# Optimization experiments

Hardware: AMD Instinct MI355X
Metric: run time of the kernel (lower is better)

The kernel has to match this reference:

```python
import jax, jax.numpy as jnp
import numpy as np
from jax.scipy.special import gammaln, logsumexp

NEG = -1e9  # finite large-negative to keep gradients NaN-free


def setup_inputs() -> dict:
    key = jax.random.key(0)
    ks = jax.random.split(key, 8)
    B, T, D, C, K = 8, 4096, 64, 32, 20
    features = jax.random.normal(ks[0], (B, T, D), dtype=jnp.float32)
    # valid lengths in [T//2, T] so every sequence is long relative to K
    lengths = jax.random.randint(ks[1], (B,), T // 2, T + 1)
    poisson_log_rates = jax.random.normal(ks[2], (C,), dtype=jnp.float32) * 0.1 + jnp.log(8.0)
    gaussian_means = jax.random.normal(ks[3], (C, D), dtype=jnp.float32) * 0.5
    # tied diagonal covariance (as produced by initialize_gaussian / tied_diag)
    gaussian_cov = jnp.diag(jax.random.uniform(ks[4], (D,), minval=0.5, maxval=1.5))
    transition_logits = jax.random.normal(ks[5], (C, C), dtype=jnp.float32) * 0.1
    init_logits = jax.random.uniform(ks[6], (C,), dtype=jnp.float32)
    return dict(features=features, poisson_log_rates=poisson_log_rates,
                gaussian_means=gaussian_means, gaussian_cov=gaussian_cov,
                transition_logits=transition_logits, init_logits=init_logits,
                lengths=lengths, max_k=K)


def reference(features, poisson_log_rates, gaussian_means, gaussian_cov,
              transition_logits, init_logits, lengths, max_k):
    B, T, D = features.shape
    C = gaussian_means.shape[0]
    K = int(max_k)

    # ---- emission log-probs: tied full-covariance Gaussian per class -> (B,T,C)
    prec = jnp.linalg.inv(gaussian_cov)
    _, logdet = jnp.linalg.slogdet(gaussian_cov)
    xP = features @ prec                                        # (B,T,D)
    quad = jnp.einsum('btd,btd->bt', xP, features)              # x^T P x
    cross = jnp.einsum('btd,cd->btc', xP, gaussian_means)       # x^T P mu
    muPmu = jnp.einsum('cd,de,ce->c', gaussian_means, prec, gaussian_means)
    const = D * jnp.log(2.0 * jnp.pi) + logdet
    emit = -0.5 * (quad[:, :, None] - 2.0 * cross + muPmu[None, None, :] + const)  # (B,T,C)

    # ---- Poisson duration scores for d = 1..K -> (K,C)
    d = jnp.arange(1, K + 1, dtype=jnp.float32)[:, None]
    length_scores = d * poisson_log_rates[None, :] - jnp.exp(poisson_log_rates)[None, :] - gammaln(d + 1.0)

    # ---- normalized transition (to <- from, softmax over 'to' axis) and init
    trans = jax.nn.log_softmax(transition_logits, axis=0)       # trans[to, from]
    init = jax.nn.log_softmax(init_logits)

    # ---- span emission sums via cumsum differences (== sliding_sum windows)
    cum = jnp.concatenate([jnp.zeros((B, 1, C), emit.dtype), jnp.cumsum(emit, axis=1)], axis=1)  # (B,T+1,C)
    t_idx = jnp.arange(1, T + 1)[:, None]                        # (T,1) span end (exclusive)
    d_idx = jnp.arange(1, K + 1)[None, :]                        # (1,K) duration
    start = jnp.clip(t_idx - d_idx, 0, None)                     # (T,K) span start
    span = cum[:, t_idx, :] - cum[:, start, :]                   # (B,T,K,C)
    seg = span + length_scores[None, None, :, :]                 # add duration scores
    seg = jnp.transpose(seg, (1, 2, 0, 3))                       # (T,K,B,C)
    dur_valid = (d_idx <= t_idx)                                 # (T,K): need d <= t
    seg = jnp.where(dur_valid[:, :, None, None], seg, NEG)

    # ---- semi-Markov forward recursion over time.
    # buf[i] = alpha_star[t-1-i]; alpha_star[s][c] = best-sum of paths ending a
    # segment at s, already including the transition into the next label c.
    buf0 = jnp.full((K, B, C), NEG, emit.dtype).at[0].set(jnp.broadcast_to(init, (B, C)))

    def step(buf, seg_t):
        alpha_t = logsumexp(buf + seg_t, axis=0)                               # (B,C)
        astar = logsumexp(alpha_t[:, None, :] + trans[None, :, :], axis=2)     # (B,C)
        buf = jnp.concatenate([astar[None], buf[:-1]], axis=0)
        return buf, alpha_t

    _, alphas = jax.lax.scan(step, buf0, seg)                    # (T,B,C)
    logZ = logsumexp(alphas[lengths - 1, jnp.arange(B), :], axis=-1)
    return -logZ  # negative log marginal likelihood per sequence
```

## Files before the change

kernel.cpp:

```cpp
#include <hip/hip_runtime.h>
#include <math.h>

#define TT 4096
#define DD 64
#define CC 32
#define KK 20
#define TPE 4128
#define L2E 1.44269504088896340736f
#define LN2f 0.69314718055994530942f
#define PIN 10.0f

#if __has_builtin(__builtin_amdgcn_permlane32_swap)
#define HAVE_PLSWAP 1
#endif
#if __has_builtin(__builtin_amdgcn_permlane16_swap)
#define HAVE_PL16 1
#endif

__device__ __align__(16) float g_pmu[32 * 64];
__device__ __align__(16) float g_p2[64];
__device__ __align__(16) float g_mc[32];
__device__ __align__(16) float g_ls2[20 * 32];
__device__ __align__(16) float g_T[32 * 32];
__device__ __align__(16) float g_init2[32];
__device__ float g_mb;
__device__ __align__(16) float g_eT[8 * 32 * TPE];

__device__ __forceinline__ float fexp2(float x) {
#if __has_builtin(__builtin_amdgcn_exp2f)
    return __builtin_amdgcn_exp2f(x);
#else
    return __exp2f(x);
#endif
}
__device__ __forceinline__ float flog2(float x) {
#if __has_builtin(__builtin_amdgcn_logf)
    return __builtin_amdgcn_logf(x);
#else
    return __log2f(x);
#endif
}

#define RF(x) __int_as_float(__builtin_amdgcn_readfirstlane(__float_as_int(x)))

__device__ __forceinline__ float xswap32(float x) {
#ifdef HAVE_PLSWAP
    int xi = __float_as_int(x);
    auto pr = __builtin_amdgcn_permlane32_swap(xi, xi, false, false);
    int r0 = ((const int*)&pr)[0];
    int r1 = ((const int*)&pr)[1];
    return (r0 == xi) ? __int_as_float(r1) : __int_as_float(r0);
#else
    return __shfl_xor(x, 32);
#endif
}
__device__ __forceinline__ float xswap16(float x) {
#ifdef HAVE_PL16
    int xi = __float_as_int(x);
    auto pr = __builtin_amdgcn_permlane16_swap(xi, xi, false, false);
    int r0 = ((const int*)&pr)[0];
    int r1 = ((const int*)&pr)[1];
    return (r0 == xi) ? __int_as_float(r1) : __int_as_float(r0);
#else
    return __shfl_xor(x, 16);
#endif
}

#define DPPF(dst, src, CTRL) \
    dst = __int_as_float(__builtin_amdgcn_update_dpp(0, __float_as_int(src), (CTRL), 0xF, 0xF, 1))

__device__ __forceinline__ float wmax64(float x) {
    float m = x, t;
    DPPF(t, m, 0xB1);  m = fmaxf(m, t);
    DPPF(t, m, 0x4E);  m = fmaxf(m, t);
    DPPF(t, m, 0x141); m = fmaxf(m, t);
    DPPF(t, m, 0x140); m = fmaxf(m, t);
    m = fmaxf(m, xswap16(m));
    m = fmaxf(m, xswap32(m));
    return m;
}

__global__ void smm_setup(const float* __restrict__ plr,
                          const float* __restrict__ mu,
                          const float* __restrict__ cov,
                          const float* __restrict__ tl,
                          const float* __restrict__ il) {
    int l = threadIdx.x;
    __shared__ float red[64];
    __shared__ float redp[64];
    __shared__ float muP[32];
    __shared__ float constc_s;
    float cd = cov[l * 64 + l];
    float pd = 1.0f / cd;
    red[l] = logf(cd);
    redp[l] = pd;
    __syncthreads();
    if (l == 0) {
        float s = 0.f;
        for (int i = 0; i < 64; ++i) s += red[i];
        constc_s = 64.0f * logf(2.0f * 3.14159265358979323846f) + s;
    }
    __syncthreads();
    float constc = constc_s;

    g_p2[l] = 0.5f * L2E * pd;
    for (int c2 = 0; c2 < 32; ++c2)
        g_pmu[c2 * 64 + l] = L2E * pd * mu[c2 * 64 + l];

    if (l < 32) {
        float s = 0.f;
        for (int d2 = 0; d2 < 64; ++d2) {
            float m_ = mu[l * 64 + d2];
            s += m_ * m_ / cov[d2 * 64 + d2];
        }
        g_mc[l] = -0.5f * L2E * (s + constc);
        muP[l] = s;
    }
    for (int idx = l; idx < KK * CC; idx += 64) {
        int k = idx >> 5, c2 = idx & 31;
        float lr = plr[c2];
        g_ls2[idx] = L2E * ((float)(k + 1) * lr - expf(lr) - lgammaf((float)(k + 2)));
    }
    if (l < 32) {
        int from = l;
        float mx = -1e30f;
        for (int to = 0; to < 32; ++to) mx = fmaxf(mx, tl[to * 32 + from]);
        float s = 0.f;
        for (int to = 0; to < 32; ++to) s += expf(tl[to * 32 + from] - mx);
        float inv = 1.0f / s;
        for (int to = 0; to < 32; ++to)
            g_T[to * 32 + from] = expf(tl[to * 32 + from] - mx) * inv;
    }
    if (l == 32) {
        float mx = -1e30f;
        for (int c2 = 0; c2 < 32; ++c2) mx = fmaxf(mx, il[c2]);
        float s = 0.f;
        for (int c2 = 0; c2 < 32; ++c2) s += expf(il[c2] - mx);
        float lse = mx + logf(s);
        for (int c2 = 0; c2 < 32; ++c2) g_init2[c2] = L2E * (il[c2] - lse);
    }
    __syncthreads();
    if (l == 0) {
        float trP = 0.f;
        for (int i = 0; i < 64; ++i) trP += redp[i];
        float mm = 0.f;
        for (int c2 = 0; c2 < 32; ++c2) mm += muP[c2];
        mm *= (1.0f / 32.0f);
        g_mb = -0.5f * L2E * (constc + trP + mm);
    }
}

__global__ __launch_bounds__(256) void smm_emit(const float* __restrict__ feat) {
    int tid = threadIdx.x;
    int c = tid & 31, tl_ = tid >> 5;
    int t = blockIdx.x * 8 + tl_;
    int b = blockIdx.y;
    const float4* x4 = (const float4*)(feat + ((size_t)b * TT + t) * DD);
    const float4* pm4 = (const float4*)(g_pmu + c * 64);
    const float4* p24 = (const float4*)g_p2;
    float acc = g_mc[c];
#pragma unroll
    for (int i = 0; i < 16; ++i) {
        float4 xv = x4[i], pm = pm4[i], pv = p24[i];
        acc = fmaf(pm.x, xv.x, acc); acc = fmaf(-pv.x * xv.x, xv.x, acc);
        acc = fmaf(pm.y, xv.y, acc); acc = fmaf(-pv.y * xv.y, xv.y, acc);
        acc = fmaf(pm.z, xv.z, acc); acc = fmaf(-pv.z * xv.z, xv.z, acc);
        acc = fmaf(pm.w, xv.w, acc); acc = fmaf(-pv.w * xv.w, xv.w, acc);
    }
    float ev = fexp2(acc - g_mb);
    __shared__ float stage[32][9];
    stage[c][tl_] = ev;
    __syncthreads();
    int c2 = tid >> 3, j = tid & 7;
    int t0 = blockIdx.x * 8;
    int ti = (t0 + j + TT - 1) & (TT - 1);
    g_eT[((size_t)b * 32 + c2) * TPE + ti] = stage[c2][j];
}

#define GMV(PF, OUT)                                                              \
    {                                                                             \
        float G1, G2, G3, G7, G15;                                                \
        DPPF(G1, PF, 0xB1); DPPF(G2, PF, 0x4E); DPPF(G3, PF, 0x1B);               \
        DPPF(G7, PF, 0x141); DPPF(G15, PF, 0x140);                                \
        float G4, G5, G6, G8, G12, G13, G14;                                      \
        DPPF(G6, G1, 0x141); DPPF(G5, G2, 0x141); DPPF(G4, G3, 0x141);            \
        DPPF(G8, G7, 0x140); DPPF(G14, G1, 0x140); DPPF(G13, G2, 0x140);          \
        DPPF(G12, G3, 0x140);                                                     \
        float G9, G10, G11;                                                       \
        DPPF(G9, G14, 0x141); DPPF(G10, G13, 0x141); DPPF(G11, G12, 0x141);       \
        float a0 = Tr[0]*(PF); a0 = fmaf(Tr[1],G1,a0);   a0 = fmaf(Tr[2],G2,a0);   a0 = fmaf(Tr[3],G3,a0);    \
        float a1 = Tr[4]*G4;   a1 = fmaf(Tr[5],G5,a1);   a1 = fmaf(Tr[6],G6,a1);   a1 = fmaf(Tr[7],G7,a1);    \
        float a2 = Tr[8]*G8;   a2 = fmaf(Tr[9],G9,a2);   a2 = fmaf(Tr[10],G10,a2); a2 = fmaf(Tr[11],G11,a2);  \
        float a3 = Tr[12]*G12; a3 = fmaf(Tr[13],G13,a3); a3 = fmaf(Tr[14],G14,a3); a3 = fmaf(Tr[15],G15,a3);  \
        float accl_ = (a0 + a1) + (a2 + a3);                                      \
        OUT = accl_ + xswap16(xswap32(accl_));                                    \
    }

#define STEPS(EV, tcur)                                                           \
    {                                                                             \
        float pf = fmaf(accf, nu, OFF);                                           \
        float naccf;                                                              \
        GMV(pf, naccf)                                                            \
        pfc = pf;                                                                 \
        if ((tcur) == lenm1) { pfL = pf; refL = refc; }                           \
        float sg = (EV) * su;                                                     \
        float u2 = accf * nu;                                                     \
        float s0 = half ? Wc : u2;                                                \
        float e9 = z9 * sg;                                                       \
        float t9 = e9 * rr;                                                       \
        float x9 = xswap32(t9);                                                   \
        float Wn = half ? x9 : t9;                                                \
        z9 = z8*sg; z8 = z7*sg; z7 = z6*sg; z6 = z5*sg; z5 = z4*sg;               \
        z4 = z3*sg; z3 = z2*sg; z2 = z1*sg; z1 = s0*sg;                           \
        float tA = Pw1*z1; tA = fmaf(Pw2,z2,tA); tA = fmaf(Pw3,z3,tA);            \
        tA = fmaf(Pw4,z4,tA); tA = fmaf(Pw5,z5,tA);                               \
        float tB = Pw6*z6; tB = fmaf(Pw7,z7,tB); tB = fmaf(Pw8,z8,tB);            \
        tB = fmaf(Pw9,z9,tB);                                                     \
        float S = tA + tB;                                                        \
        float Sx = xswap32(S);                                                    \
        OFF = fmaxf((S + Sx) + Wn, 1e-36f);                                       \
        nu = sg * E1;                                                             \
        accf = naccf;                                                             \
        Wc = Wn;                                                                  \
        refc += (double)r8;                                                       \
    }

#define STEPM(EV)                                                                 \
    {                                                                             \
        float pf = fmaf(accf, nu, OFF);                                           \
        float naccf;                                                              \
        GMV(pf, naccf)                                                            \
        pfc = pf;                                                                 \
        float sg = (EV) * su;                                                     \
        float u2 = accf * nu;                                                     \
        float s0 = half ? Wc : u2;                                                \
        float e9 = z9 * sg;                                                       \
        float t9 = e9 * rr;                                                       \
        float x9 = xswap32(t9);                                                   \
        float Wn = half ? x9 : t9;                                                \
        z9 = z8*sg; z8 = z7*sg; z7 = z6*sg; z6 = z5*sg; z5 = z4*sg;               \
        z4 = z3*sg; z3 = z2*sg; z2 = z1*sg; z1 = s0*sg;                           \
        float tA = Pw1*z1; tA = fmaf(Pw2,z2,tA); tA = fmaf(Pw3,z3,tA);            \
        tA = fmaf(Pw4,z4,tA); tA = fmaf(Pw5,z5,tA);                               \
        float tB = Pw6*z6; tB = fmaf(Pw7,z7,tB); tB = fmaf(Pw8,z8,tB);            \
        tB = fmaf(Pw9,z9,tB);                                                     \
        float S = tA + tB;                                                        \
        float Sx = xswap32(S);                                                    \
        OFF = fmaxf((S + Sx) + Wn, 1e-36f);                                       \
        nu = sg * E1;                                                             \
        accf = naccf;                                                             \
        Wc = Wn;                                                                  \
    }

#define CTRLDB(gain)                                                              \
    {                                                                             \
        float err = flog2(wmax64(pfc)) + PIN;                                     \
        err = fminf(fmaxf(err, -50.0f), 50.0f);                                   \
        float cs = fexp2(-err);                                                   \
        accf *= cs; OFF *= cs; Wc *= cs;                                          \
        z1*=cs; z2*=cs; z3*=cs; z4*=cs; z5*=cs;                                   \
        z6*=cs; z7*=cs; z8*=cs; z9*=cs;                                           \
        refc += (double)err;                                                      \
        r8 = fmaf(err, (gain), r8);                                               \
        su = fexp2(mb - r8);                                                      \
    }

#define CTRL4M(gain)                                                              \
    {                                                                             \
        float err = flog2(wmax64(pfc)) + PIN;                                     \
        err = fminf(fmaxf(err, -50.0f), 50.0f);                                   \
        float cs = fexp2(-err);                                                   \
        accf *= cs; OFF *= cs; Wc *= cs;                                          \
        z1*=cs; z2*=cs; z3*=cs; z4*=cs; z5*=cs;                                   \
        z6*=cs; z7*=cs; z8*=cs; z9*=cs;                                           \
        refc += (double)err + (double)(4.0f * r8);                                \
        r8 = fmaf(err, (gain), r8);                                               \
        su = fexp2(mb - r8);                                                      \
    }

__global__ __launch_bounds__(64, 1)
void smm_forward(const int* __restrict__ lens, float* __restrict__ out) {
    const int b = blockIdx.x;
    const int l = threadIdx.x;
    const int c = l & 31;
    const int half = l >> 5;
    const int i16 = l & 15;
    const int rb = ((l >> 4) & 1) * 16;
    const int cT = half ? (c ^ 16) : c;

    float lsr[10];
#pragma unroll
    for (int i = 0; i < 10; ++i) lsr[i] = g_ls2[(half * 10 + i) * 32 + c];

    float Tr[16];
#pragma unroll
    for (int j2 = 0; j2 < 16; ++j2) Tr[j2] = g_T[cT * 32 + rb + (i16 ^ j2)];

    float tswp = __shfl_xor(lsr[0], 32);
    float ls1c = half ? tswp : lsr[0];
    float d11s = half ? lsr[0] : tswp;

    float Pw1 = fexp2(lsr[1] - lsr[0]), Pw2 = fexp2(lsr[2] - lsr[0]);
    float Pw3 = fexp2(lsr[3] - lsr[0]), Pw4 = fexp2(lsr[4] - lsr[0]);
    float Pw5 = fexp2(lsr[5] - lsr[0]), Pw6 = fexp2(lsr[6] - lsr[0]);
    float Pw7 = fexp2(lsr[7] - lsr[0]), Pw8 = fexp2(lsr[8] - lsr[0]);
    float Pw9 = fexp2(lsr[9] - lsr[0]);
    float rr  = fexp2(d11s - lsr[0]);
    float E1  = fexp2(ls1c);

    int len = lens[b];
    if (len < 16) len = 16;
    if (len > TT) len = TT;
    const int lenm1 = len - 1;
    const int tb_end = lenm1 & ~7;

    const float* eT = g_eT + ((size_t)b * 32 + c) * TPE;
    const float4* cp = (const float4*)eT;
    float4 cA = cp[0], cB = cp[1], pA = cp[2], pB = cp[3];

    float mb = g_mb;
    float e0 = eT[TT - 1];
    float iv = g_init2[c] + ls1c;
    float a0v = iv + mb + flog2(fmaxf(e0, 1e-37f));
    float refc0 = wmax64(a0v);
    double refc = (double)refc0;
    float nu = e0 * fexp2(iv + mb - refc0 - PIN);
    float accf = 1.0f, OFF = 0.0f;
    float z1=0.f,z2=0.f,z3=0.f,z4=0.f,z5=0.f,z6=0.f,z7=0.f,z8=0.f,z9=0.f;
    float Wc = 0.f;
    float r8 = mb;
    float su = 1.0f;
    float pfL = 0.f, pfc = 0.f;
    double refL = 0.0;

    {
        float4 nA = cp[4], nB = cp[5];
        STEPS(cA.x, 0) CTRLDB(0.3f) STEPS(cA.y, 1) CTRLDB(0.3f)
        STEPS(cA.z, 2) CTRLDB(0.3f) STEPS(cA.w, 3) CTRLDB(0.3f)
        STEPS(cB.x, 4) CTRLDB(0.3f) STEPS(cB.y, 5) CTRLDB(0.3f)
        STEPS(cB.z, 6) CTRLDB(0.3f) STEPS(cB.w, 7) CTRLDB(0.3f)
        cA = pA; cB = pB; pA = nA; pB = nB;
    }

    for (int tb = 8; tb < tb_end; tb += 8) {
        int bi = tb >> 2;
        float4 nA = cp[bi + 4], nB = cp[bi + 5];
        STEPM(cA.x) STEPM(cA.y) STEPM(cA.z) STEPM(cA.w)
        CTRL4M(0.125f)
        STEPM(cB.x) STEPM(cB.y) STEPM(cB.z) STEPM(cB.w)
        CTRL4M(0.125f)
        cA = pA; cB = pB; pA = nA; pB = nB;
    }

    STEPS(cA.x, tb_end + 0) STEPS(cA.y, tb_end + 1)
    STEPS(cA.z, tb_end + 2) STEPS(cA.w, tb_end + 3)
    STEPS(cB.x, tb_end + 4) STEPS(cB.y, tb_end + 5)
    STEPS(cB.z, tb_end + 6) STEPS(cB.w, tb_end + 7)

    float tot = pfL;
#pragma unroll
    for (int st = 1; st < 32; st <<= 1) tot += __shfl_xor(tot, st);
    if (l == 0) {
        double a = refL + (double)PIN + (double)flog2(fmaxf(tot, 1e-37f));
        out[b] = (float)(-0.69314718055994530942 * a);
    }
}

extern "C" void kernel_launch(void* const* d_in, const int* in_sizes, int n_in,
                              void* d_out, int out_size, void* d_ws, size_t ws_size,
                              hipStream_t stream) {
    const float* feat = (const float*)d_in[0];
    const float* plr  = (const float*)d_in[1];
    const float* mu   = (const float*)d_in[2];
    const float* cov  = (const float*)d_in[3];
    const float* tl   = (const float*)d_in[4];
    const float* il   = (const float*)d_in[5];
    const int*   lens = (const int*)d_in[6];
    float* outf = (float*)d_out;
    int B = in_sizes[6];
    if (B > 8) B = 8;

    smm_setup<<<1, 64, 0, stream>>>(plr, mu, cov, tl, il);
    smm_emit<<<dim3(TT / 8, B), 256, 0, stream>>>(feat);
    smm_forward<<<B, 64, 0, stream>>>(lens, outf);
}
```

Measured before the change: 768.9 us.

## Fuse two recursion steps per iteration with packed v2 duration-window math

Replaces the single-step STEPM recursion with a two-step STEP2 that unrolls the shifting z-window algebraically. It computes both steps' duration sums from the same stored window using packed 2-wide FMAs (v_pk_fma). The window is stored as four v2 registers plus z9, which roughly halves shift and scale work per time step. The aim is to shorten the serial dependency chain and the instruction count of the hot loop. The cost is more register pressure and a reordering of floating-point operations that could shift rounding.

```diff
diff --git a/kernel.cpp b/kernel.cpp
--- a/kernel.cpp
+++ b/kernel.cpp
@@ -9,6 +9,8 @@
 #define L2E 1.44269504088896340736f
 #define LN2f 0.69314718055994530942f
 #define PIN 10.0f
+
+typedef float v2 __attribute__((ext_vector_type(2)));
 
 #if __has_builtin(__builtin_amdgcn_permlane32_swap)
 #define HAVE_PLSWAP 1
@@ -225,31 +227,48 @@
         refc += (double)r8;                                                       \
     }
 
-#define STEPM(EV)                                                                 \
+#define STEP2(EVA, EVB)                                                           \
     {                                                                             \
-        float pf = fmaf(accf, nu, OFF);                                           \
-        float naccf;                                                              \
-        GMV(pf, naccf)                                                            \
-        pfc = pf;                                                                 \
-        float sg = (EV) * su;                                                     \
-        float u2 = accf * nu;                                                     \
-        float s0 = half ? Wc : u2;                                                \
-        float e9 = z9 * sg;                                                       \
-        float t9 = e9 * rr;                                                       \
-        float x9 = xswap32(t9);                                                   \
-        float Wn = half ? x9 : t9;                                                \
-        z9 = z8*sg; z8 = z7*sg; z7 = z6*sg; z6 = z5*sg; z5 = z4*sg;               \
-        z4 = z3*sg; z3 = z2*sg; z2 = z1*sg; z1 = s0*sg;                           \
-        float tA = Pw1*z1; tA = fmaf(Pw2,z2,tA); tA = fmaf(Pw3,z3,tA);            \
-        tA = fmaf(Pw4,z4,tA); tA = fmaf(Pw5,z5,tA);                               \
-        float tB = Pw6*z6; tB = fmaf(Pw7,z7,tB); tB = fmaf(Pw8,z8,tB);            \
-        tB = fmaf(Pw9,z9,tB);                                                     \
-        float S = tA + tB;                                                        \
-        float Sx = xswap32(S);                                                    \
-        OFF = fmaxf((S + Sx) + Wn, 1e-36f);                                       \
-        nu = sg * E1;                                                             \
-        accf = naccf;                                                             \
-        Wc = Wn;                                                                  \
+        float pfA = fmaf(accf, nu, OFF);                                          \
+        float naccfA;                                                             \
+        GMV(pfA, naccfA)                                                          \
+        pfc = pfA;                                                                \
+        float sgA = (EVA) * su;                                                   \
+        float u2A = accf * nu;                                                    \
+        float s0A = half ? Wc : u2A;                                              \
+        float t9A = (z9 * sgA) * rr;                                              \
+        float x9A = xswap32(t9A);                                                 \
+        float WnA = half ? x9A : t9A;                                             \
+        v2 dB = PwB1 * P1;                                                        \
+        dB = __builtin_elementwise_fma(PwB2, P2, dB);                             \
+        dB = __builtin_elementwise_fma(PwB3, P3, dB);                             \
+        dB = __builtin_elementwise_fma(PwB4, P4, dB);                             \
+        float SA = sgA * fmaf(Pw1, s0A, dB.x + dB.y);                             \
+        float OFFB = fmaxf((SA + xswap32(SA)) + WnA, 1e-36f);                     \
+        float nuB = sgA * E1;                                                     \
+        float pfB = fmaf(naccfA, nuB, OFFB);                                      \
+        float naccfB;                                                             \
+        GMV(pfB, naccfB)                                                          \
+        float sgB = (EVB) * su;                                                   \
+        float ss = sgA * sgB;                                                     \
+        float u2B = naccfA * nuB;                                                 \
+        float s0B = half ? WnA : u2B;                                             \
+        float t9B = (P4.y * ss) * rr;                                             \
+        float x9B = xswap32(t9B);                                                 \
+        float WnB = half ? x9B : t9B;                                             \
+        v2 dC = PwC1 * P1;                                                        \
+        dC = __builtin_elementwise_fma(PwC2, P2, dC);                             \
+        dC = __builtin_elementwise_fma(PwC3, P3, dC);                             \
+        dC = __builtin_elementwise_fma(PwC4, P4, dC);                             \
+        float innerB = fmaf(Pw2, s0A, dC.x + dC.y);                               \
+        float SB = sgB * fmaf(sgA, innerB, Pw1 * s0B);                            \
+        float OFFn = fmaxf((SB + xswap32(SB)) + WnB, 1e-36f);                     \
+        v2 ssv = {ss, ss};                                                        \
+        z9 = P4.x * ss;                                                           \
+        P4 = P3 * ssv; P3 = P2 * ssv; P2 = P1 * ssv;                              \
+        v2 nP1; nP1.x = s0B * sgB; nP1.y = s0A * ss;                              \
+        P1 = nP1;                                                                 \
+        OFF = OFFn; nu = sgB * E1; accf = naccfB; Wc = WnB;                       \
     }
 
 #define CTRLDB(gain)                                                              \
@@ -265,14 +284,14 @@
         su = fexp2(mb - r8);                                                      \
     }
 
-#define CTRL4M(gain)                                                              \
+#define CTRL2M(gain)                                                              \
     {                                                                             \
         float err = flog2(wmax64(pfc)) + PIN;                                     \
         err = fminf(fmaxf(err, -50.0f), 50.0f);                                   \
         float cs = fexp2(-err);                                                   \
-        accf *= cs; OFF *= cs; Wc *= cs;                                          \
-        z1*=cs; z2*=cs; z3*=cs; z4*=cs; z5*=cs;                                   \
-        z6*=cs; z7*=cs; z8*=cs; z9*=cs;                                           \
+        v2 csv = {cs, cs};                                                        \
+        accf *= cs; OFF *= cs; Wc *= cs; z9 *= cs;                                \
+        P1 *= csv; P2 *= csv; P3 *= csv; P4 *= csv;                               \
         refc += (double)err + (double)(4.0f * r8);                                \
         r8 = fmaf(err, (gain), r8);                                               \
         su = fexp2(mb - r8);                                                      \
@@ -307,6 +326,9 @@
     float Pw9 = fexp2(lsr[9] - lsr[0]);
     float rr  = fexp2(d11s - lsr[0]);
     float E1  = fexp2(ls1c);
+
+    v2 PwB1 = {Pw2, Pw3}, PwB2 = {Pw4, Pw5}, PwB3 = {Pw6, Pw7}, PwB4 = {Pw8, Pw9};
+    v2 PwC1 = {Pw3, Pw4}, PwC2 = {Pw5, Pw6}, PwC3 = {Pw7, Pw8}, PwC4 = {Pw9, 0.0f};
 
     int len = lens[b];
     if (len < 16) len = 16;
@@ -332,6 +354,7 @@
     float su = 1.0f;
     float pfL = 0.f, pfc = 0.f;
     double refL = 0.0;
+    v2 P1, P2, P3, P4;
 
     {
         float4 nA = cp[4], nB = cp[5];
@@ -342,16 +365,20 @@
         cA = pA; cB = pB; pA = nA; pB = nB;
     }
 
+    P1 = (v2){z1, z2}; P2 = (v2){z3, z4}; P3 = (v2){z5, z6}; P4 = (v2){z7, z8};
+
     for (int tb = 8; tb < tb_end; tb += 8) {
         int bi = tb >> 2;
         float4 nA = cp[bi + 4], nB = cp[bi + 5];
-        STEPM(cA.x) STEPM(cA.y) STEPM(cA.z) STEPM(cA.w)
-        CTRL4M(0.125f)
-        STEPM(cB.x) STEPM(cB.y) STEPM(cB.z) STEPM(cB.w)
-        CTRL4M(0.125f)
+        STEP2(cA.x, cA.y) STEP2(cA.z, cA.w)
+        CTRL2M(0.125f)
+        STEP2(cB.x, cB.y) STEP2(cB.z, cB.w)
+        CTRL2M(0.125f)
         cA = pA; cB = pB; pA = nA; pB = nB;
     }
 
+    z1 = P1.x; z2 = P1.y; z3 = P2.x; z4 = P2.y;
+    z5 = P3.x; z6 = P3.y; z7 = P4.x; z8 = P4.y;
     STEPS(cA.x, tb_end + 0) STEPS(cA.y, tb_end + 1)
     STEPS(cA.z, tb_end + 2) STEPS(cA.w, tb_end + 3)
     STEPS(cB.x, tb_end + 4) STEPS(cB.y, tb_end + 5)
```

After: 764.5 us. No clear change (-0.6%).
